# Kernel optimization log

Hardware: AMD Instinct MI355X
Metric: run time of the kernel (lower is better)

The kernel has to match this reference:

```python
import jax, jax.numpy as jnp
import numpy as np

THRESHOLD = 0.2  # relation_threshold default
LN_EPS = 1e-5


def setup_inputs() -> dict:
    key = jax.random.key(0)
    ks = jax.random.split(key, 4)
    N1, N2, F, H, R = 256, 256, 512, 512, 4
    feats_img = jax.random.normal(ks[0], (N1, F), dtype=jnp.float32)
    feats_txt = jax.random.normal(ks[1], (N2, F), dtype=jnp.float32)
    # relation_projector params (R stacked copies of the 2-layer MLP)
    W1 = jax.random.normal(ks[2], (R, H, 2 * F), dtype=jnp.float32) / np.sqrt(2 * F)
    b1 = jnp.zeros((R, H), dtype=jnp.float32)
    gamma = jnp.ones((R, H), dtype=jnp.float32)
    beta = jnp.zeros((R, H), dtype=jnp.float32)
    w2 = jax.random.normal(ks[3], (R, H), dtype=jnp.float32) / np.sqrt(H)
    b2 = jnp.zeros((R,), dtype=jnp.float32)
    return {"feats_img": feats_img, "feats_txt": feats_txt, "W1": W1, "b1": b1,
            "gamma": gamma, "beta": beta, "w2": w2, "b2": b2}


def _relation_scores(x, W1, b1, gamma, beta, w2, b2):
    """Vectorized pairwise MLP: for each relation r, score[i,j] = MLP_r(cat(x_i, x_j)).
    Returns [N, N, R]."""
    N, F = x.shape
    R = W1.shape[0]
    Wl, Wr = W1[:, :, :F], W1[:, :, F:]  # Linear on concat = left half @ x_i + right half @ x_j
    scores = []
    for r in range(R):  # small fixed loop over relations keeps peak memory at one [N,N,H] block
        a = x @ Wl[r].T                                  # [N, H]
        b = x @ Wr[r].T                                  # [N, H]
        h = a[:, None, :] + b[None, :, :] + b1[r]        # [N, N, H]
        mu = h.mean(-1, keepdims=True)
        var = h.var(-1, keepdims=True)                   # biased var, matches torch LayerNorm
        hn = (h - mu) * jax.lax.rsqrt(var + LN_EPS) * gamma[r] + beta[r]
        s = jnp.maximum(hn, 0.0) @ w2[r] + b2[r]         # [N, N]
        scores.append(s)
    return jnp.stack(scores, axis=-1)                    # [N, N, R]


def reference(feats_img, feats_txt, W1, b1, gamma, beta, w2, b2):
    # node_features = cat over modalities (node_types is a static host-side list: omitted)
    x = jnp.concatenate([feats_img, feats_txt], axis=0)  # [N, F]
    S = _relation_scores(x, W1, b1, gamma, beta, w2, b2) # [N, N, R]
    best_rel = jnp.argmax(S, axis=-1).astype(jnp.int32)  # edge_types, dense form
    best_score = S.max(axis=-1)                          # edge_weights, dense form
    N = x.shape[0]
    diag = jnp.eye(N, dtype=bool)
    edge_mask = (~diag) & (best_score > THRESHOLD)       # dense encoding of edge_index
    return x, best_score, best_rel, edge_mask
```

## Files before the change

kernel.cpp:

```cpp
#include <hip/hip_runtime.h>
#include <math.h>


namespace {
constexpr size_t PLANE  = 512 * 512;
constexpr size_t OFF_A   = 0;
constexpr size_t OFF_B   = OFF_A + 4 * PLANE;
constexpr size_t OFF_DOT = OFF_B + 4 * PLANE;
constexpr size_t OFF_S   = OFF_DOT + 8 * PLANE;
constexpr size_t OFF_MA  = OFF_S + 8 * PLANE;
constexpr size_t OFF_QA  = OFF_MA + 2048;
constexpr size_t OFF_MB  = OFF_QA + 2048;
constexpr size_t OFF_QB  = OFF_MB + 2048;
constexpr size_t OFF_GBW = OFF_QB + 2048;
}

__global__ __launch_bounds__(256) void k0_gemm(const float* __restrict__ img,
                                               const float* __restrict__ txt,
                                               const float* __restrict__ W1,
                                               const float* __restrict__ b1,
                                               float* __restrict__ ws) {
  const int b = blockIdx.x;
  const int it = b >> 6;
  const int ct = b & 63;
  const int which = ct >> 5;
  const int r = (ct >> 3) & 3;
  const int ht = ct & 7;
  const int i0 = it << 6, h0 = ht << 6;
  const int t = threadIdx.x;
  const int tx = t & 15, ty = t >> 4;

  __shared__ float Xs[16 * 68];
  __shared__ float Wsm[16 * 68];

  float acc[16], pacc[16];
#pragma unroll
  for (int p = 0; p < 16; ++p) { acc[p] = 0.f; pacc[p] = 0.f; }

  const int srow = t >> 2;
  const int sf4 = (t & 3) << 2;
  const int xi = i0 + srow;
  const float* xrow = (xi < 256) ? (img + (size_t)xi * 512)
                                 : (txt + (size_t)(xi - 256) * 512);
  const float* wrow = W1 + (size_t)(r * 512 + h0 + srow) * 1024 + which * 512;

  for (int k0 = 0; k0 < 512; k0 += 16) {
    const float4 xv = *(const float4*)(xrow + k0 + sf4);
    const float4 wv = *(const float4*)(wrow + k0 + sf4);
    __syncthreads();
    Xs[(sf4 + 0) * 68 + srow] = xv.x;
    Xs[(sf4 + 1) * 68 + srow] = xv.y;
    Xs[(sf4 + 2) * 68 + srow] = xv.z;
    Xs[(sf4 + 3) * 68 + srow] = xv.w;
    Wsm[(sf4 + 0) * 68 + srow] = wv.x;
    Wsm[(sf4 + 1) * 68 + srow] = wv.y;
    Wsm[(sf4 + 2) * 68 + srow] = wv.z;
    Wsm[(sf4 + 3) * 68 + srow] = wv.w;
    __syncthreads();
#pragma unroll
    for (int k = 0; k < 16; ++k) {
      const float4 a4 = *(const float4*)&Xs[k * 68 + 4 * ty];
      const float4 b4 = *(const float4*)&Wsm[k * 68 + 4 * tx];
      const float av[4] = {a4.x, a4.y, a4.z, a4.w};
      const float bv[4] = {b4.x, b4.y, b4.z, b4.w};
#pragma unroll
      for (int c = 0; c < 4; ++c)
#pragma unroll
        for (int d = 0; d < 4; ++d)
          pacc[c * 4 + d] = fmaf(av[c], bv[d], pacc[c * 4 + d]);
    }
#pragma unroll
    for (int p = 0; p < 16; ++p) { acc[p] += pacc[p]; pacc[p] = 0.f; }
  }

  float4 bb = make_float4(0.f, 0.f, 0.f, 0.f);
  if (which) bb = *(const float4*)(b1 + r * 512 + h0 + 4 * tx);
  float* dst = ws + (which ? OFF_B : OFF_A) + (size_t)r * PLANE;
#pragma unroll
  for (int c = 0; c < 4; ++c) {
    float4 v;
    v.x = acc[c * 4 + 0] + bb.x;
    v.y = acc[c * 4 + 1] + bb.y;
    v.z = acc[c * 4 + 2] + bb.z;
    v.w = acc[c * 4 + 3] + bb.w;
    *(float4*)(dst + (size_t)(i0 + 4 * ty + c) * 512 + h0 + 4 * tx) = v;
  }
}

__global__ __launch_bounds__(256) void k1_stats(float* __restrict__ ws,
                                                const float* __restrict__ gamma,
                                                const float* __restrict__ beta,
                                                const float* __restrict__ w2) {
  const int t = threadIdx.x;
  const int gw = (blockIdx.x * 256 + t) >> 6;
  const int lane = t & 63;
  const int which = gw >> 11;
  const int rr = (gw >> 9) & 3;
  const int row = gw & 511;
  const float* src =
      ws + (which ? OFF_B : OFF_A) + (size_t)(rr * 512 + row) * 512 + lane * 8;
  float s = 0.f, q = 0.f;
#pragma unroll
  for (int c = 0; c < 2; ++c) {
    const float4 v = *(const float4*)(src + c * 4);
    s += v.x + v.y + v.z + v.w;
    q += v.x * v.x + v.y * v.y + v.z * v.z + v.w * v.w;
  }
#pragma unroll
  for (int off = 32; off >= 1; off >>= 1) {
    s += __shfl_down(s, off, 64);
    q += __shfl_down(q, off, 64);
  }
  if (lane == 0) {
    ws[(which ? OFF_MB : OFF_MA) + rr * 512 + row] = s * (1.f / 512.f);
    ws[(which ? OFF_QB : OFF_QA) + rr * 512 + row] = q;
  }
  if (blockIdx.x < 8) {
    const int idx = blockIdx.x * 256 + t;
    float4 g;
    g.x = gamma[idx]; g.y = beta[idx]; g.z = w2[idx]; g.w = 0.f;
    *(float4*)(ws + OFF_GBW + (size_t)idx * 4) = g;
  }
}

__global__ __launch_bounds__(256) void k2_dot(float* __restrict__ ws) {
  const int b = blockIdx.x;
  const int jt = b & 7, it = (b >> 3) & 7, r = (b >> 6) & 3, ks = b >> 8;
  const int i0 = it << 6, j0 = jt << 6;
  const int kb = ks << 8;
  const int t = threadIdx.x;
  const int tx = t & 15, ty = t >> 4;

  __shared__ float As[16 * 68];
  __shared__ float Bs[16 * 68];

  float acc[16];
#pragma unroll
  for (int p = 0; p < 16; ++p) acc[p] = 0.f;

  const int srow = t >> 2, sf4 = (t & 3) << 2;
  const float* arow = ws + OFF_A + (size_t)(r * 512 + i0 + srow) * 512 + kb;
  const float* brow = ws + OFF_B + (size_t)(r * 512 + j0 + srow) * 512 + kb;

  for (int k0 = 0; k0 < 256; k0 += 16) {
    const float4 av = *(const float4*)(arow + k0 + sf4);
    const float4 bv = *(const float4*)(brow + k0 + sf4);
    __syncthreads();
    As[(sf4 + 0) * 68 + srow] = av.x;
    As[(sf4 + 1) * 68 + srow] = av.y;
    As[(sf4 + 2) * 68 + srow] = av.z;
    As[(sf4 + 3) * 68 + srow] = av.w;
    Bs[(sf4 + 0) * 68 + srow] = bv.x;
    Bs[(sf4 + 1) * 68 + srow] = bv.y;
    Bs[(sf4 + 2) * 68 + srow] = bv.z;
    Bs[(sf4 + 3) * 68 + srow] = bv.w;
    __syncthreads();
#pragma unroll
    for (int k = 0; k < 16; ++k) {
      const float4 a4 = *(const float4*)&As[k * 68 + 4 * ty];
      const float4 b4 = *(const float4*)&Bs[k * 68 + 4 * tx];
      const float av2[4] = {a4.x, a4.y, a4.z, a4.w};
      const float bv2[4] = {b4.x, b4.y, b4.z, b4.w};
#pragma unroll
      for (int c = 0; c < 4; ++c)
#pragma unroll
        for (int d = 0; d < 4; ++d)
          acc[c * 4 + d] = fmaf(av2[c], bv2[d], acc[c * 4 + d]);
    }
  }
  float* dst = ws + OFF_DOT + (size_t)ks * (4 * PLANE) + (size_t)r * PLANE;
#pragma unroll
  for (int c = 0; c < 4; ++c) {
    float4 v;
    v.x = acc[c * 4 + 0]; v.y = acc[c * 4 + 1];
    v.z = acc[c * 4 + 2]; v.w = acc[c * 4 + 3];
    *(float4*)(dst + (size_t)(i0 + 4 * ty + c) * 512 + j0 + 4 * tx) = v;
  }
}

__global__ __launch_bounds__(512) void k3_score(float* __restrict__ ws) {
  const int b = blockIdx.x;
  const int jt = b & 7, it = (b >> 3) & 7, r = (b >> 6) & 3, ks = b >> 8;
  const int i0 = it << 6, j0 = jt << 6;
  const int t = threadIdx.x;
  const int tx = t & 31, ty = t >> 5;

  __shared__ float As2[64 * 65];
  __shared__ float Bs2[64 * 65];
  __shared__ float gsS[64 * 4];

  const float4 mav = *(const float4*)(ws + OFF_MA + r * 512 + i0 + 4 * ty);
  const float4 qav = *(const float4*)(ws + OFF_QA + r * 512 + i0 + 4 * ty);
  const float2 mbv = *(const float2*)(ws + OFF_MB + r * 512 + j0 + 2 * tx);
  const float2 qbv = *(const float2*)(ws + OFF_QB + r * 512 + j0 + 2 * tx);
  const float mavA[4] = {mav.x, mav.y, mav.z, mav.w};
  const float qavA[4] = {qav.x, qav.y, qav.z, qav.w};
  const float mbA[2] = {mbv.x, mbv.y};
  const float qbA[2] = {qbv.x, qbv.y};
  float Sv[8], Tv[8], acc[8];
#pragma unroll
  for (int c = 0; c < 4; ++c) {
    const size_t doff = (size_t)r * PLANE + (size_t)(i0 + 4 * ty + c) * 512 + j0 + 2 * tx;
    const float2 d0 = *(const float2*)(ws + OFF_DOT + doff);
    const float2 d1 = *(const float2*)(ws + OFF_DOT + 4 * PLANE + doff);
    const float dA[2] = {d0.x + d1.x, d0.y + d1.y};
#pragma unroll
    for (int d = 0; d < 2; ++d) {
      const int p = c * 2 + d;
      const float mu = mavA[c] + mbA[d];
      const float msq = (qavA[c] + qbA[d] + 2.f * dA[d]) * (1.f / 512.f);
      const float var = msq - mu * mu;
      const float sv = 1.0f / sqrtf(var + 1e-5f);
      Sv[p] = sv;
      Tv[p] = -mu * sv;
      acc[p] = 0.f;
    }
  }

  const int kbase = ks << 8;
  const int srow = t >> 4, sf4 = (t & 15) << 2;
  for (int kc = 0; kc < 4; ++kc) {
    const int kb = kbase + (kc << 6);
    float4 avs[2], bvs[2];
#pragma unroll
    for (int c2 = 0; c2 < 2; ++c2) {
      avs[c2] = *(const float4*)(ws + OFF_A +
                 (size_t)(r * 512 + i0 + srow + 32 * c2) * 512 + kb + sf4);
      bvs[c2] = *(const float4*)(ws + OFF_B +
                 (size_t)(r * 512 + j0 + srow + 32 * c2) * 512 + kb + sf4);
    }
    float4 gv = make_float4(0.f, 0.f, 0.f, 0.f);
    if (t < 64) gv = *(const float4*)(ws + OFF_GBW + (size_t)(r * 512 + kb + t) * 4);
    __syncthreads();
#pragma unroll
    for (int c2 = 0; c2 < 2; ++c2) {
      const int row = srow + 32 * c2;
      As2[row * 65 + sf4 + 0] = avs[c2].x;
      As2[row * 65 + sf4 + 1] = avs[c2].y;
      As2[row * 65 + sf4 + 2] = avs[c2].z;
      As2[row * 65 + sf4 + 3] = avs[c2].w;
      Bs2[row * 65 + sf4 + 0] = bvs[c2].x;
      Bs2[row * 65 + sf4 + 1] = bvs[c2].y;
      Bs2[row * 65 + sf4 + 2] = bvs[c2].z;
      Bs2[row * 65 + sf4 + 3] = bvs[c2].w;
    }
    if (t < 64) *(float4*)(gsS + t * 4) = gv;
    __syncthreads();

    float cacc[8];
#pragma unroll
    for (int p = 0; p < 8; ++p) cacc[p] = 0.f;

#pragma unroll 4
    for (int k = 0; k < 64; ++k) {
      const float4 g = *(const float4*)(gsS + 4 * k);
      float aA[4], bB[2];
#pragma unroll
      for (int c = 0; c < 4; ++c) aA[c] = As2[(4 * ty + c) * 65 + k];
#pragma unroll
      for (int d = 0; d < 2; ++d) bB[d] = Bs2[(2 * tx + d) * 65 + k];
#pragma unroll
      for (int c = 0; c < 4; ++c)
#pragma unroll
        for (int d = 0; d < 2; ++d) {
          const int p = c * 2 + d;
          const float u = aA[c] + bB[d];
          const float pp = fmaf(u, Sv[p], Tv[p]);
          const float hn = fmaf(pp, g.x, g.y);
          const float m = fmaxf(hn, 0.f);
          cacc[p] = fmaf(m, g.z, cacc[p]);
        }
    }
#pragma unroll
    for (int p = 0; p < 8; ++p) acc[p] += cacc[p];
  }

  float* dst = ws + OFF_S + (size_t)ks * (4 * PLANE) + (size_t)r * PLANE;
#pragma unroll
  for (int c = 0; c < 4; ++c) {
    float2 v;
    v.x = acc[c * 2 + 0];
    v.y = acc[c * 2 + 1];
    *(float2*)(dst + (size_t)(i0 + 4 * ty + c) * 512 + j0 + 2 * tx) = v;
  }
}

__global__ __launch_bounds__(256) void k4_combine(const float* __restrict__ ws,
                                                  const float* __restrict__ img,
                                                  const float* __restrict__ txt,
                                                  const float* __restrict__ b2,
                                                  float* __restrict__ out) {
  const int idx = blockIdx.x * 256 + threadIdx.x;
  const int i = idx >> 9, j = idx & 511;
  const float* s0 = ws + OFF_S;
  const float* s1 = ws + OFF_S + 4 * PLANE;
  float best = -3.4e38f;
  int rel = 0;
#pragma unroll
  for (int r = 0; r < 4; ++r) {
    const float s = s0[r * PLANE + idx] + s1[r * PLANE + idx] + b2[r];
    if (s > best) { best = s; rel = r; }
  }
  out[idx] = (i < 256) ? img[idx] : txt[idx - 131072];
  out[PLANE + idx] = best;
  out[2 * PLANE + idx] = (float)rel;
  out[3 * PLANE + idx] = (i != j && (double)best > 0.2) ? 1.0f : 0.0f;
}

extern "C" void kernel_launch(void* const* d_in, const int* in_sizes, int n_in,
                              void* d_out, int out_size, void* d_ws, size_t ws_size,
                              hipStream_t stream) {
  const float* img   = (const float*)d_in[0];
  const float* txt   = (const float*)d_in[1];
  const float* W1    = (const float*)d_in[2];
  const float* b1    = (const float*)d_in[3];
  const float* gamma = (const float*)d_in[4];
  const float* beta  = (const float*)d_in[5];
  const float* w2    = (const float*)d_in[6];
  const float* b2    = (const float*)d_in[7];
  float* ws  = (float*)d_ws;
  float* out = (float*)d_out;
  (void)in_sizes; (void)n_in; (void)out_size; (void)ws_size;

  hipLaunchKernelGGL(k0_gemm,    dim3(512),  dim3(256), 0, stream, img, txt, W1, b1, ws);
  hipLaunchKernelGGL(k1_stats,   dim3(1024), dim3(256), 0, stream, ws, gamma, beta, w2);
  hipLaunchKernelGGL(k2_dot,     dim3(512),  dim3(256), 0, stream, ws);
  hipLaunchKernelGGL(k3_score,   dim3(512),  dim3(512), 0, stream, ws);
  hipLaunchKernelGGL(k4_combine, dim3(1024), dim3(256), 0, stream, ws, img, txt, b2, out);
}
```

Before: 195.7 us.

## Rewrite ReLU-dot as abs identity and retile score kernel with swizzled LDS

The score kernel now writes ReLU(h)·w as 0.5·w·h + 0.5·|w·h|. The linear part is precomputed per row in the stats kernel as a rank-1 term, plus a per-relation constant added in combine. The inner loop shrinks to three FMAs plus an abs per element, with a sign factor standing in for the ReLU max. The kernel also moves to 256 threads with a 4x4 register tile, float4 LDS reads and an XOR-swizzled shared layout instead of padding. This cuts ALU work and LDS traffic per pair, at the cost of more registers per thread and fewer threads per block.

Result: slower. 207.1 us (+5.8%).

```diff
diff --git a/kernel.cpp b/kernel.cpp
--- a/kernel.cpp
+++ b/kernel.cpp
@@ -10,9 +10,14 @@
 constexpr size_t OFF_S   = OFF_DOT + 8 * PLANE;
 constexpr size_t OFF_MA  = OFF_S + 8 * PLANE;
 constexpr size_t OFF_QA  = OFF_MA + 2048;
-constexpr size_t OFF_MB  = OFF_QA + 2048;
+constexpr size_t OFF_PAp = OFF_QA + 2048;
+constexpr size_t OFF_MB  = OFF_PAp + 2048;
 constexpr size_t OFF_QB  = OFF_MB + 2048;
-constexpr size_t OFF_GBW = OFF_QB + 2048;
+constexpr size_t OFF_PBp = OFF_QB + 2048;
+constexpr size_t OFF_P   = OFF_PBp + 2048;
+constexpr size_t OFF_Q   = OFF_P + 2048;
+constexpr size_t OFF_SG  = OFF_Q + 2048;
+constexpr size_t OFF_QSP = OFF_SG + 2048;
 }
 
 __global__ __launch_bounds__(256) void k0_gemm(const float* __restrict__ img,
@@ -91,6 +96,7 @@
                                                 const float* __restrict__ gamma,
                                                 const float* __restrict__ beta,
                                                 const float* __restrict__ w2) {
+  __shared__ float red[4];
   const int t = threadIdx.x;
   const int gw = (blockIdx.x * 256 + t) >> 6;
   const int lane = t & 63;
@@ -99,27 +105,52 @@
   const int row = gw & 511;
   const float* src =
       ws + (which ? OFF_B : OFF_A) + (size_t)(rr * 512 + row) * 512 + lane * 8;
-  float s = 0.f, q = 0.f;
+  const float* gp = gamma + rr * 512 + lane * 8;
+  const float* wp = w2 + rr * 512 + lane * 8;
+  float s = 0.f, q = 0.f, pa = 0.f, gg = 0.f;
 #pragma unroll
   for (int c = 0; c < 2; ++c) {
     const float4 v = *(const float4*)(src + c * 4);
-    s += v.x + v.y + v.z + v.w;
-    q += v.x * v.x + v.y * v.y + v.z * v.z + v.w * v.w;
+    const float4 g = *(const float4*)(gp + c * 4);
+    const float4 w = *(const float4*)(wp + c * 4);
+    const float vv[4] = {v.x, v.y, v.z, v.w};
+    const float gv[4] = {g.x, g.y, g.z, g.w};
+    const float wv[4] = {w.x, w.y, w.z, w.w};
+#pragma unroll
+    for (int e = 0; e < 4; ++e) {
+      const float p = 0.5f * gv[e] * wv[e];
+      s += vv[e];
+      q += vv[e] * vv[e];
+      pa += p * vv[e];
+      gg += p;
+    }
   }
 #pragma unroll
   for (int off = 32; off >= 1; off >>= 1) {
     s += __shfl_down(s, off, 64);
     q += __shfl_down(q, off, 64);
+    pa += __shfl_down(pa, off, 64);
+    gg += __shfl_down(gg, off, 64);
   }
   if (lane == 0) {
-    ws[(which ? OFF_MB : OFF_MA) + rr * 512 + row] = s * (1.f / 512.f);
+    const float ma = s * (1.f / 512.f);
+    ws[(which ? OFF_MB : OFF_MA) + rr * 512 + row] = ma;
     ws[(which ? OFF_QB : OFF_QA) + rr * 512 + row] = q;
+    ws[(which ? OFF_PBp : OFF_PAp) + rr * 512 + row] = pa - ma * gg;
   }
   if (blockIdx.x < 8) {
     const int idx = blockIdx.x * 256 + t;
-    float4 g;
-    g.x = gamma[idx]; g.y = beta[idx]; g.z = w2[idx]; g.w = 0.f;
-    *(float4*)(ws + OFF_GBW + (size_t)idx * 4) = g;
+    const float g = gamma[idx], be = beta[idx], w = w2[idx];
+    const float qv = 0.5f * be * w;
+    ws[OFF_P + idx] = 0.5f * g * w;
+    ws[OFF_Q + idx] = qv;
+    ws[OFF_SG + idx] = copysignf(1.f, w);
+    float qs = qv;
+#pragma unroll
+    for (int off = 32; off >= 1; off >>= 1) qs += __shfl_down(qs, off, 64);
+    if (lane == 0) red[t >> 6] = qs;
+    __syncthreads();
+    if (t == 0) ws[OFF_QSP + blockIdx.x] = red[0] + red[1] + red[2] + red[3];
   }
 }
 
@@ -178,110 +209,134 @@
   }
 }
 
-__global__ __launch_bounds__(512) void k3_score(float* __restrict__ ws) {
+__global__ __launch_bounds__(256) void k3_score(float* __restrict__ ws) {
   const int b = blockIdx.x;
   const int jt = b & 7, it = (b >> 3) & 7, r = (b >> 6) & 3, ks = b >> 8;
   const int i0 = it << 6, j0 = jt << 6;
   const int t = threadIdx.x;
-  const int tx = t & 31, ty = t >> 5;
-
-  __shared__ float As2[64 * 65];
-  __shared__ float Bs2[64 * 65];
-  __shared__ float gsS[64 * 4];
+  const int tx = t & 15, ty = t >> 4;
+
+  __shared__ float As[64 * 64];
+  __shared__ float Bs[64 * 64];
+  __shared__ float Pl[3 * 64];
 
   const float4 mav = *(const float4*)(ws + OFF_MA + r * 512 + i0 + 4 * ty);
   const float4 qav = *(const float4*)(ws + OFF_QA + r * 512 + i0 + 4 * ty);
-  const float2 mbv = *(const float2*)(ws + OFF_MB + r * 512 + j0 + 2 * tx);
-  const float2 qbv = *(const float2*)(ws + OFF_QB + r * 512 + j0 + 2 * tx);
-  const float mavA[4] = {mav.x, mav.y, mav.z, mav.w};
-  const float qavA[4] = {qav.x, qav.y, qav.z, qav.w};
-  const float mbA[2] = {mbv.x, mbv.y};
-  const float qbA[2] = {qbv.x, qbv.y};
-  float Sv[8], Tv[8], acc[8];
-#pragma unroll
-  for (int c = 0; c < 4; ++c) {
-    const size_t doff = (size_t)r * PLANE + (size_t)(i0 + 4 * ty + c) * 512 + j0 + 2 * tx;
-    const float2 d0 = *(const float2*)(ws + OFF_DOT + doff);
-    const float2 d1 = *(const float2*)(ws + OFF_DOT + 4 * PLANE + doff);
-    const float dA[2] = {d0.x + d1.x, d0.y + d1.y};
-#pragma unroll
-    for (int d = 0; d < 2; ++d) {
-      const int p = c * 2 + d;
-      const float mu = mavA[c] + mbA[d];
-      const float msq = (qavA[c] + qbA[d] + 2.f * dA[d]) * (1.f / 512.f);
+  const float4 pav = *(const float4*)(ws + OFF_PAp + r * 512 + i0 + 4 * ty);
+  const float4 mbv = *(const float4*)(ws + OFF_MB + r * 512 + j0 + 4 * tx);
+  const float4 qbv = *(const float4*)(ws + OFF_QB + r * 512 + j0 + 4 * tx);
+  const float4 pbv = *(const float4*)(ws + OFF_PBp + r * 512 + j0 + 4 * tx);
+  const float maA[4] = {mav.x, mav.y, mav.z, mav.w};
+  const float qaA[4] = {qav.x, qav.y, qav.z, qav.w};
+  const float paA[4] = {pav.x, pav.y, pav.z, pav.w};
+  const float mbA[4] = {mbv.x, mbv.y, mbv.z, mbv.w};
+  const float qbA[4] = {qbv.x, qbv.y, qbv.z, qbv.w};
+  const float pbA[4] = {pbv.x, pbv.y, pbv.z, pbv.w};
+
+  float Sv[16], Tv[16], acc[16];
+#pragma unroll
+  for (int c = 0; c < 4; ++c) {
+    const size_t doff =
+        (size_t)r * PLANE + (size_t)(i0 + 4 * ty + c) * 512 + j0 + 4 * tx;
+    const float4 d0 = *(const float4*)(ws + OFF_DOT + doff);
+    const float4 d1 = *(const float4*)(ws + OFF_DOT + 4 * PLANE + doff);
+    const float dA[4] = {d0.x + d1.x, d0.y + d1.y, d0.z + d1.z, d0.w + d1.w};
+#pragma unroll
+    for (int d = 0; d < 4; ++d) {
+      const int p = c * 4 + d;
+      const float mu = maA[c] + mbA[d];
+      const float msq = (qaA[c] + qbA[d] + 2.f * dA[d]) * (1.f / 512.f);
       const float var = msq - mu * mu;
       const float sv = 1.0f / sqrtf(var + 1e-5f);
       Sv[p] = sv;
       Tv[p] = -mu * sv;
-      acc[p] = 0.f;
-    }
+      acc[p] = ks ? 0.f : sv * (paA[c] + pbA[d]);
+    }
+  }
+
+  int aoff[4], boff[4];
+#pragma unroll
+  for (int c = 0; c < 4; ++c) {
+    const int row = 4 * ty + c;
+    aoff[c] = row * 256 + (((row + (row >> 2)) & 15) << 4);
+  }
+#pragma unroll
+  for (int d = 0; d < 4; ++d) {
+    const int row = 4 * tx + d;
+    boff[d] = row * 256 + (((row + (row >> 2)) & 15) << 4);
   }
 
   const int kbase = ks << 8;
-  const int srow = t >> 4, sf4 = (t & 15) << 2;
   for (int kc = 0; kc < 4; ++kc) {
     const int kb = kbase + (kc << 6);
-    float4 avs[2], bvs[2];
-#pragma unroll
-    for (int c2 = 0; c2 < 2; ++c2) {
-      avs[c2] = *(const float4*)(ws + OFF_A +
-                 (size_t)(r * 512 + i0 + srow + 32 * c2) * 512 + kb + sf4);
-      bvs[c2] = *(const float4*)(ws + OFF_B +
-                 (size_t)(r * 512 + j0 + srow + 32 * c2) * 512 + kb + sf4);
-    }
-    float4 gv = make_float4(0.f, 0.f, 0.f, 0.f);
-    if (t < 64) gv = *(const float4*)(ws + OFF_GBW + (size_t)(r * 512 + kb + t) * 4);
-    __syncthreads();
-#pragma unroll
-    for (int c2 = 0; c2 < 2; ++c2) {
-      const int row = srow + 32 * c2;
-      As2[row * 65 + sf4 + 0] = avs[c2].x;
-      As2[row * 65 + sf4 + 1] = avs[c2].y;
-      As2[row * 65 + sf4 + 2] = avs[c2].z;
-      As2[row * 65 + sf4 + 3] = avs[c2].w;
-      Bs2[row * 65 + sf4 + 0] = bvs[c2].x;
-      Bs2[row * 65 + sf4 + 1] = bvs[c2].y;
-      Bs2[row * 65 + sf4 + 2] = bvs[c2].z;
-      Bs2[row * 65 + sf4 + 3] = bvs[c2].w;
-    }
-    if (t < 64) *(float4*)(gsS + t * 4) = gv;
-    __syncthreads();
-
-    float cacc[8];
-#pragma unroll
-    for (int p = 0; p < 8; ++p) cacc[p] = 0.f;
+    float4 ag[4], bg[4], pg;
+#pragma unroll
+    for (int m = 0; m < 4; ++m) {
+      ag[m] = *(const float4*)(ws + OFF_A +
+               (size_t)(r * 512 + i0 + ty + 16 * m) * 512 + kb + 4 * tx);
+      bg[m] = *(const float4*)(ws + OFF_B +
+               (size_t)(r * 512 + j0 + ty + 16 * m) * 512 + kb + 4 * tx);
+    }
+    if (t < 48) {
+      const size_t po = (t < 16) ? OFF_P : ((t < 32) ? OFF_Q : OFF_SG);
+      pg = *(const float4*)(ws + po + r * 512 + kb + 4 * (t & 15));
+    }
+    __syncthreads();
+#pragma unroll
+    for (int m = 0; m < 4; ++m) {
+      const int row = ty + 16 * m;
+      const int sw = (row + (row >> 2)) & 15;
+      *(float4*)((char*)As + row * 256 + ((tx ^ sw) << 4)) = ag[m];
+      *(float4*)((char*)Bs + row * 256 + ((tx ^ sw) << 4)) = bg[m];
+    }
+    if (t < 48) *(float4*)((char*)Pl + t * 16) = pg;
+    __syncthreads();
 
 #pragma unroll 4
-    for (int k = 0; k < 64; ++k) {
-      const float4 g = *(const float4*)(gsS + 4 * k);
-      float aA[4], bB[2];
-#pragma unroll
-      for (int c = 0; c < 4; ++c) aA[c] = As2[(4 * ty + c) * 65 + k];
-#pragma unroll
-      for (int d = 0; d < 2; ++d) bB[d] = Bs2[(2 * tx + d) * 65 + k];
+    for (int k4 = 0; k4 < 16; ++k4) {
+      const float4 Pk = *(const float4*)((char*)Pl + (k4 << 4));
+      const float4 Qk = *(const float4*)((char*)Pl + 256 + (k4 << 4));
+      const float4 Sk = *(const float4*)((char*)Pl + 512 + (k4 << 4));
+      float4 av[4], bv[4];
 #pragma unroll
       for (int c = 0; c < 4; ++c)
-#pragma unroll
-        for (int d = 0; d < 2; ++d) {
-          const int p = c * 2 + d;
-          const float u = aA[c] + bB[d];
-          const float pp = fmaf(u, Sv[p], Tv[p]);
-          const float hn = fmaf(pp, g.x, g.y);
-          const float m = fmaxf(hn, 0.f);
-          cacc[p] = fmaf(m, g.z, cacc[p]);
-        }
-    }
-#pragma unroll
-    for (int p = 0; p < 8; ++p) acc[p] += cacc[p];
+        av[c] = *(const float4*)((char*)As + (aoff[c] ^ (k4 << 4)));
+#pragma unroll
+      for (int d = 0; d < 4; ++d)
+        bv[d] = *(const float4*)((char*)Bs + (boff[d] ^ (k4 << 4)));
+#pragma unroll
+      for (int kk = 0; kk < 4; ++kk) {
+        const float pk = ((const float*)&Pk)[kk];
+        const float qk = ((const float*)&Qk)[kk];
+        const float sk = ((const float*)&Sk)[kk];
+        float aa[4], bb[4];
+#pragma unroll
+        for (int c = 0; c < 4; ++c) aa[c] = ((const float*)&av[c])[kk];
+#pragma unroll
+        for (int d = 0; d < 4; ++d) bb[d] = ((const float*)&bv[d])[kk];
+#pragma unroll
+        for (int c = 0; c < 4; ++c)
+#pragma unroll
+          for (int d = 0; d < 4; ++d) {
+            const int p = c * 4 + d;
+            const float u = aa[c] + bb[d];
+            const float t1 = fmaf(u, Sv[p], Tv[p]);
+            const float h = fmaf(t1, pk, qk);
+            acc[p] = fmaf(fabsf(h), sk, acc[p]);
+          }
+      }
+    }
   }
 
   float* dst = ws + OFF_S + (size_t)ks * (4 * PLANE) + (size_t)r * PLANE;
 #pragma unroll
   for (int c = 0; c < 4; ++c) {
-    float2 v;
-    v.x = acc[c * 2 + 0];
-    v.y = acc[c * 2 + 1];
-    *(float2*)(dst + (size_t)(i0 + 4 * ty + c) * 512 + j0 + 2 * tx) = v;
+    float4 v;
+    v.x = acc[c * 4 + 0];
+    v.y = acc[c * 4 + 1];
+    v.z = acc[c * 4 + 2];
+    v.w = acc[c * 4 + 3];
+    *(float4*)(dst + (size_t)(i0 + 4 * ty + c) * 512 + j0 + 4 * tx) = v;
   }
 }
 
@@ -294,11 +349,13 @@
   const int i = idx >> 9, j = idx & 511;
   const float* s0 = ws + OFF_S;
   const float* s1 = ws + OFF_S + 4 * PLANE;
+  const float* qsp = ws + OFF_QSP;
   float best = -3.4e38f;
   int rel = 0;
 #pragma unroll
   for (int r = 0; r < 4; ++r) {
-    const float s = s0[r * PLANE + idx] + s1[r * PLANE + idx] + b2[r];
+    const float cr = b2[r] + qsp[2 * r] + qsp[2 * r + 1];
+    const float s = s0[r * PLANE + idx] + s1[r * PLANE + idx] + cr;
     if (s > best) { best = s; rel = r; }
   }
   out[idx] = (i < 256) ? img[idx] : txt[idx - 131072];
@@ -325,6 +382,6 @@
   hipLaunchKernelGGL(k0_gemm,    dim3(512),  dim3(256), 0, stream, img, txt, W1, b1, ws);
   hipLaunchKernelGGL(k1_stats,   dim3(1024), dim3(256), 0, stream, ws, gamma, beta, w2);
   hipLaunchKernelGGL(k2_dot,     dim3(512),  dim3(256), 0, stream, ws);
-  hipLaunchKernelGGL(k3_score,   dim3(512),  dim3(512), 0, stream, ws);
+  hipLaunchKernelGGL(k3_score,   dim3(512),  dim3(256), 0, stream, ws);
   hipLaunchKernelGGL(k4_combine, dim3(1024), dim3(256), 0, stream, ws, img, txt, b2, out);
 }
```
